# Kernel optimization log

Hardware: AMD Instinct MI355X
Metric: run time of the kernel (lower is better)

The kernel has to match this reference:

```python
import jax, jax.numpy as jnp
from jax import lax
import numpy as np

B, N, C = 64, 8732, 81  # batch, anchors (SSD300), classes (COCO+bg)
POS_RATE = 0.003        # keep 3*num_pos < N (argsort column index must be in range)


def setup_inputs() -> dict:
    key = jax.random.key(0)
    k1, k2, k3, k4, k5, k6 = jax.random.split(key, 6)
    pred_conf = jax.random.normal(k1, (B, N, C), dtype=jnp.float32)
    pred_loc = jax.random.normal(k2, (B, N, 4), dtype=jnp.float32)
    # one-hot gt_conf; class 0 = background; sparse positives
    is_pos = jax.random.uniform(k3, (B, N)) < POS_RATE
    labels = jnp.where(is_pos, jax.random.randint(k4, (B, N), 1, C), 0)
    gt_conf = jax.nn.one_hot(labels, C, dtype=jnp.float32)
    gt_loc = jax.random.normal(k5, (B, N, 4), dtype=jnp.float32)
    return {"pred_conf": pred_conf, "pred_loc": pred_loc,
            "gt_conf": gt_conf, "gt_loc": gt_loc}


def reference(pred_conf, pred_loc, gt_conf, gt_loc):
    negative_ratio = 3.0
    # softmax cross entropy per anchor: [B, N]
    log_sm = jax.nn.log_softmax(pred_conf, axis=-1)
    conf_loss = -jnp.sum(log_sm * gt_conf, axis=-1)

    # positive mask (gt background prob == 0 => positive); detached in original
    pos_mask = (lax.stop_gradient(gt_conf)[:, :, 0] == 0).astype(jnp.float32)
    num_pos = jnp.sum(pos_mask)
    positive_conf_loss = pos_mask * conf_loss

    # hard-negative mining (faithful to original, including the quirk that the
    # "threshold" is the argsort INDEX value at column num_negative_conf)
    neg_mask = 1.0 - pos_mask
    cl_neg = lax.stop_gradient(conf_loss) * neg_mask  # detached in original
    order = jnp.argsort(cl_neg, axis=-1)              # [B, N] ascending
    num_neg = (negative_ratio * num_pos).astype(jnp.int32)  # scalar, traced
    idx = jnp.broadcast_to(num_neg, (cl_neg.shape[0], 1))
    thr = jnp.take_along_axis(order, idx, axis=1).astype(jnp.float32)  # [B,1]
    neg_mask = neg_mask * (cl_neg > thr).astype(jnp.float32)
    negative_conf_loss = neg_mask * conf_loss

    conf_total = jnp.sum(positive_conf_loss + negative_conf_loss, axis=-1)  # [B]

    # smooth-L1-ish loc loss (faithful, incl. loc_loss_mask == linear mask bug)
    d = pred_loc - gt_loc
    lin = (jnp.abs(lax.stop_gradient(d)) > 1.0).astype(jnp.float32)
    loc = ((jnp.abs(d) - 0.5) * lin + 0.5 * d * d * (1.0 - lin)) * lin
    loc_total = jnp.sum(loc, axis=(-1, -2))  # [B]

    return conf_total, loc_total
```

## Files before the change

### kernel.cpp

```cpp
#include <hip/hip_runtime.h>
#include <math.h>

#define NCLS 81
#define NANCH 8732
#define NB 64
#define BUCKET_STRIDE 16
#define HSTRIDE 257
#define NLOC_BLK  2240
#define NCONF_BLK 1792
#define NTILES 17464
#define TILE_A 32
#define WAVE_F 648

__global__ __launch_bounds__(256) void conf_loc_kernel(
    const float* __restrict__ pred_conf,
    const float* __restrict__ gt_conf,
    const float* __restrict__ pred_loc,
    const float* __restrict__ gt_loc,
    float* __restrict__ cl_out,
    int* __restrict__ pos_buckets,
    float* __restrict__ row_pos,
    float* __restrict__ locp)
{
    __shared__ float sx[2][2592];
    __shared__ int labels[2][32];
    __shared__ float red[4];

    const int tid = threadIdx.x;
    const int lane = tid & 63, w = tid >> 6;

    if (blockIdx.x < NLOC_BLK) {
        const int bid = blockIdx.x;
        const int b = bid & 63;
        const int chunk = bid >> 6;
        const int idx = chunk * 256 + tid;
        float local = 0.f;
        if (idx < NANCH) {
            const float4* p = (const float4*)(pred_loc + (size_t)b * (NANCH * 4));
            const float4* g = (const float4*)(gt_loc + (size_t)b * (NANCH * 4));
            float4 pv = p[idx];
            float4 gv = g[idx];
            float a0 = fabsf(pv.x - gv.x), a1 = fabsf(pv.y - gv.y);
            float a2 = fabsf(pv.z - gv.z), a3 = fabsf(pv.w - gv.w);
            local  = (a0 > 1.f) ? (a0 - 0.5f) : 0.f;
            local += (a1 > 1.f) ? (a1 - 0.5f) : 0.f;
            local += (a2 > 1.f) ? (a2 - 0.5f) : 0.f;
            local += (a3 > 1.f) ? (a3 - 0.5f) : 0.f;
        }
        for (int off = 32; off; off >>= 1) local += __shfl_xor(local, off);
        if (lane == 0) red[w] = local;
        __syncthreads();
        if (tid == 0) locp[bid] = red[0] + red[1] + red[2] + red[3];
        return;
    }

    const int pid = blockIdx.x - NLOC_BLK;
    float* swA = &sx[0][w * WAVE_F];
    float* swB = &sx[1][w * WAVE_F];
    int pacc = 0;

#define DMA3(dst, src)                                                              \
    do {                                                                            \
        __builtin_amdgcn_global_load_lds(                                           \
            (const __attribute__((address_space(1))) unsigned int*)((src) + lane),  \
            (__attribute__((address_space(3))) unsigned int*)(&(dst)[lane * 4]),    \
            16, 0, 0);                                                              \
        __builtin_amdgcn_global_load_lds(                                           \
            (const __attribute__((address_space(1))) unsigned int*)((src) + 64 + lane), \
            (__attribute__((address_space(3))) unsigned int*)(&(dst)[(64 + lane) * 4]), \
            16, 0, 0);                                                              \
        if (lane < 34)                                                              \
            __builtin_amdgcn_global_load_lds(                                       \
                (const __attribute__((address_space(1))) unsigned int*)((src) + 128 + lane), \
                (__attribute__((address_space(3))) unsigned int*)(&(dst)[(128 + lane) * 4]), \
                16, 0, 0);                                                          \
    } while (0)

    int T = pid;
    {
        const float4* ps = (const float4*)(pred_conf + (size_t)T * 2592 + w * WAVE_F);
        DMA3(swA, ps);
    }
    const float4* gs = (const float4*)(gt_conf + (size_t)T * 2592 + w * WAVE_F);
    float4 g0 = gs[lane];
    float4 g1 = gs[64 + lane];
    float4 g2 = (lane < 34) ? gs[128 + lane] : float4{0.f, 0.f, 0.f, 0.f};

    int cur = 0;
    for (;;) {
        const int Tn = T + NCONF_BLK;
        const bool hasN = (Tn < NTILES);
        float* swc = cur ? swB : swA;
        float* swn = cur ? swA : swB;

        if (hasN) {
            const float4* ps = (const float4*)(pred_conf + (size_t)Tn * 2592 + w * WAVE_F);
            DMA3(swn, ps);
            asm volatile("s_waitcnt vmcnt(3)" ::: "memory");
        } else {
            asm volatile("s_waitcnt vmcnt(0)" ::: "memory");
        }
        __builtin_amdgcn_sched_barrier(0);

        {
            const float4 gg[3] = {g0, g1, g2};
#pragma unroll
            for (int c = 0; c < 3; ++c) {
                const int f4 = c * 64 + lane;
                float gv[4] = {gg[c].x, gg[c].y, gg[c].z, gg[c].w};
#pragma unroll
                for (int t = 0; t < 4; ++t) {
                    if (gv[t] != 0.0f) {
                        const int e = 4 * f4 + t;
                        const int a = e / 81, cls = e - 81 * a;
                        labels[cur][w * 8 + a] = cls;
                        pacc += (cls != 0);
                    }
                }
            }
        }
        if (hasN) {
            const float4* gn = (const float4*)(gt_conf + (size_t)Tn * 2592 + w * WAVE_F);
            g0 = gn[lane];
            g1 = gn[64 + lane];
            g2 = (lane < 34) ? gn[128 + lane] : float4{0.f, 0.f, 0.f, 0.f};
        }
        asm volatile("s_waitcnt lgkmcnt(0)" ::: "memory");
        __builtin_amdgcn_sched_barrier(0);

        {
            const int a = lane >> 3, r = lane & 7;
            const float* xr = swc + a * 81;
            float s = 0.f;
#pragma unroll
            for (int j = 0; j < 10; ++j) s += __expf(xr[r + 8 * j]);
            if (r == 0) s += __expf(xr[80]);
            s += __shfl_xor(s, 1);
            s += __shfl_xor(s, 2);
            s += __shfl_xor(s, 4);
            const float lse = __logf(s);

            const int anchor = T * TILE_A + w * 8 + a;
            float contrib = 0.f;
            if (r == 0) {
                const int lbl = labels[cur][w * 8 + a];
                const float cl = lse - xr[lbl];
                const bool posf = (lbl != 0);
                cl_out[anchor] = posf ? 0.0f : cl;
                if (posf) contrib = cl;
            }
            const int b = anchor / NANCH;
            const int bF = __builtin_amdgcn_readfirstlane(b);
            float c0 = (b == bF) ? contrib : 0.0f;
            float c1 = contrib - c0;
            for (int off = 32; off; off >>= 1) {
                c0 += __shfl_xor(c0, off);
                c1 += __shfl_xor(c1, off);
            }
            if (lane == 0) {
                if (c0 != 0.f) atomicAdd(&row_pos[bF], c0);
                if (c1 != 0.f) atomicAdd(&row_pos[bF + 1], c1);
            }
        }

        if (!hasN) break;
        T = Tn;
        cur ^= 1;
    }
#undef DMA3

    for (int off = 32; off; off >>= 1) pacc += __shfl_xor(pacc, off);
    if (lane == 0 && pacc)
        atomicAdd(&pos_buckets[(((pid << 2) | w) & 63) * BUCKET_STRIDE], pacc);
}

__global__ __launch_bounds__(1024) void select_kernel(
    const float* __restrict__ val,
    const int* __restrict__ pos_buckets,
    const float* __restrict__ row_pos,
    const float* __restrict__ locp,
    float* __restrict__ out)
{
    __shared__ float cl[NANCH];
    __shared__ int hist[4 * HSTRIDE];
    __shared__ int wsum[16];
    __shared__ float fred[16];
    __shared__ int sh_numpos;
    __shared__ unsigned int sh_prefix;
    __shared__ int sh_k, sh_thr;

    const int b = blockIdx.x;
    const int tid = threadIdx.x;
    const int lane = tid & 63, w = tid >> 6;
    const int hofs = (w & 3) * HSTRIDE;
    const float* row = val + b * NANCH;

    if (tid < 64) {
        int v = pos_buckets[tid * BUCKET_STRIDE];
        for (int off = 32; off; off >>= 1) v += __shfl_xor(v, off);
        if (tid == 0) sh_numpos = v;
    } else if (tid < 128) {
        float v = (lane < 35) ? locp[lane * 64 + b] : 0.f;
        for (int off = 32; off; off >>= 1) v += __shfl_xor(v, off);
        if (lane == 0) out[64 + b] = v;
    }
    for (int i = tid; i < NANCH; i += 1024) cl[i] = row[i];
    __syncthreads();

    int k = 3 * sh_numpos;
    if (k > NANCH - 1) k = NANCH - 1;
    if (k < 0) k = 0;

    unsigned int prefix = 0u;
    for (int r = 0; r < 4; ++r) {
        const int shift = 24 - 8 * r;
        const unsigned int maskHigh = (r == 0) ? 0u : (0xFFFFFFFFu << (shift + 8));
        for (int j = tid; j < 4 * HSTRIDE; j += 1024) hist[j] = 0;
        __syncthreads();
        if (r == 0) {
            for (int i0 = 0; i0 < 9216; i0 += 1024) {
                int i = i0 + tid;
                bool valid = (i < NANCH);
                unsigned int u = valid ? __float_as_uint(cl[i]) : 0u;
                int bin = (int)(u >> 24);
                unsigned long long act = __ballot(valid);
                while (act) {
                    int leader = (int)__ffsll((long long)act) - 1;
                    int lbin = __shfl(bin, leader);
                    unsigned long long sm = __ballot(valid && (bin == lbin));
                    if (lane == leader) atomicAdd(&hist[hofs + lbin], (int)__popcll(sm));
                    act &= ~sm;
                }
            }
        } else {
            for (int i = tid; i < NANCH; i += 1024) {
                unsigned int u = __float_as_uint(cl[i]);
                if ((u & maskHigh) == prefix)
                    atomicAdd(&hist[hofs + ((u >> shift) & 0xFF)], 1);
            }
        }
        __syncthreads();
        int h = 0, v = 0;
        if (tid < 256) {
            h = hist[tid] + hist[HSTRIDE + tid] + hist[2 * HSTRIDE + tid]
              + hist[3 * HSTRIDE + tid];
            v = h;
#pragma unroll
            for (int off = 1; off < 64; off <<= 1) {
                int u2 = __shfl_up(v, off);
                if (lane >= off) v += u2;
            }
            if (lane == 63) wsum[w] = v;
        }
        __syncthreads();
        if (tid < 256) {
            int add = 0;
            for (int i = 0; i < w; ++i) add += wsum[i];
            int incl = v + add, excl = incl - h;
            if (excl <= k && k < incl) {
                sh_prefix = prefix | ((unsigned int)tid << shift);
                sh_k = k - excl;
            }
        }
        __syncthreads();
        prefix = sh_prefix;
        k = sh_k;
        __syncthreads();
    }
    const unsigned int T = prefix;

    const int CHUNK = 9;
    int lo = tid * CHUNK; if (lo > NANCH) lo = NANCH;
    int hi = lo + CHUNK; if (hi > NANCH) hi = NANCH;
    int cnt = 0;
    for (int i = lo; i < hi; ++i)
        cnt += (__float_as_uint(cl[i]) == T);
    int v2 = cnt;
#pragma unroll
    for (int off = 1; off < 64; off <<= 1) {
        int u2 = __shfl_up(v2, off);
        if (lane >= off) v2 += u2;
    }
    if (lane == 63) wsum[w] = v2;
    __syncthreads();
    if (tid < 16) {
        int s = wsum[tid];
#pragma unroll
        for (int off = 1; off < 16; off <<= 1) {
            int u2 = __shfl_up(s, off);
            if (lane >= off) s += u2;
        }
        wsum[tid] = s;
    }
    __syncthreads();
    {
        int add = (w == 0) ? 0 : wsum[w - 1];
        int incl = v2 + add, excl = incl - cnt;
        if (excl <= k && k < incl) {
            int need = k - excl, idx = NANCH - 1;
            for (int i = lo; i < hi; ++i) {
                if (__float_as_uint(cl[i]) == T) {
                    if (need == 0) { idx = i; break; }
                    --need;
                }
            }
            sh_thr = idx;
        }
    }
    __syncthreads();

    const float thr = (float)sh_thr;
    float local = 0.f;
    for (int i = tid; i < NANCH; i += 1024) {
        float c = cl[i];
        if (c > thr) local += c;
    }
    for (int off = 32; off; off >>= 1) local += __shfl_xor(local, off);
    if (lane == 0) fred[w] = local;
    __syncthreads();
    if (tid == 0) {
        float t = row_pos[b];
        for (int i = 0; i < 16; ++i) t += fred[i];
        out[b] = t;
    }
}

extern "C" void kernel_launch(void* const* d_in, const int* in_sizes, int n_in,
                              void* d_out, int out_size, void* d_ws, size_t ws_size,
                              hipStream_t stream) {
    const float* pred_conf = (const float*)d_in[0];
    const float* pred_loc  = (const float*)d_in[1];
    const float* gt_conf   = (const float*)d_in[2];
    const float* gt_loc    = (const float*)d_in[3];
    float* out = (float*)d_out;

    int*   pos_buckets = (int*)d_ws;
    float* row_pos     = (float*)((char*)d_ws + 4096);
    float* locp        = (float*)((char*)d_ws + 5120);
    float* vals        = (float*)((char*)d_ws + 16384);

    hipMemsetAsync(d_ws, 0, 8192, stream);

    conf_loc_kernel<<<NLOC_BLK + NCONF_BLK, 256, 0, stream>>>(
        pred_conf, gt_conf, pred_loc, gt_loc, vals, pos_buckets, row_pos, locp);
    select_kernel<<<NB, 1024, 0, stream>>>(vals, pos_buckets, row_pos, locp, out);
}
```

Baseline: 393.3 us.

## Fuse conf/loc and selection kernels via a global completion counter

Merges the two kernel launches into one grid. The last 64 blocks spin on a global atomic done-counter until all producer blocks have finished, then run the per-row radix select with 256 threads instead of 1024. This removes one kernel launch and the gap between the two kernels. In exchange it relies on the waiting blocks not starving producers (they are scheduled last), and each selection block now has 4x fewer threads for the histogram passes.

```diff
diff --git a/kernel.cpp b/kernel.cpp
--- a/kernel.cpp
+++ b/kernel.cpp
@@ -8,11 +8,33 @@
 #define HSTRIDE 257
 #define NLOC_BLK  2240
 #define NCONF_BLK 1792
+#define NSEL_BLK  64
 #define NTILES 17464
 #define TILE_A 32
 #define WAVE_F 648
-
-__global__ __launch_bounds__(256) void conf_loc_kernel(
+#define DONE_TARGET (NLOC_BLK + NCONF_BLK)
+
+#define ALD_I(p) __hip_atomic_load((p), __ATOMIC_RELAXED, __HIP_MEMORY_SCOPE_AGENT)
+#define ALD_F(p) __hip_atomic_load((p), __ATOMIC_RELAXED, __HIP_MEMORY_SCOPE_AGENT)
+
+struct ConfSh {
+    float sx[2][2592];
+    int labels[2][32];
+    float red[4];
+};
+struct SelSh {
+    float cl[NANCH];
+    int hist[4 * HSTRIDE];
+    int wsum[4];
+    float fred[4];
+    int numpos;
+    unsigned int prefix;
+    int k;
+    int thr;
+};
+union ShMem { ConfSh c; SelSh s; };
+
+__global__ __launch_bounds__(256) void fused_kernel(
     const float* __restrict__ pred_conf,
     const float* __restrict__ gt_conf,
     const float* __restrict__ pred_loc,
@@ -20,11 +42,11 @@
     float* __restrict__ cl_out,
     int* __restrict__ pos_buckets,
     float* __restrict__ row_pos,
-    float* __restrict__ locp)
+    float* __restrict__ locp,
+    int* __restrict__ done,
+    float* __restrict__ out)
 {
-    __shared__ float sx[2][2592];
-    __shared__ int labels[2][32];
-    __shared__ float red[4];
+    __shared__ ShMem sh;
 
     const int tid = threadIdx.x;
     const int lane = tid & 63, w = tid >> 6;
@@ -48,16 +70,21 @@
             local += (a3 > 1.f) ? (a3 - 0.5f) : 0.f;
         }
         for (int off = 32; off; off >>= 1) local += __shfl_xor(local, off);
-        if (lane == 0) red[w] = local;
-        __syncthreads();
-        if (tid == 0) locp[bid] = red[0] + red[1] + red[2] + red[3];
+        if (lane == 0) sh.c.red[w] = local;
+        __syncthreads();
+        if (tid == 0) {
+            locp[bid] = sh.c.red[0] + sh.c.red[1] + sh.c.red[2] + sh.c.red[3];
+            __threadfence();
+            atomicAdd(done, 1);
+        }
         return;
     }
 
-    const int pid = blockIdx.x - NLOC_BLK;
-    float* swA = &sx[0][w * WAVE_F];
-    float* swB = &sx[1][w * WAVE_F];
-    int pacc = 0;
+    if (blockIdx.x < NLOC_BLK + NCONF_BLK) {
+        const int pid = blockIdx.x - NLOC_BLK;
+        float* swA = &sh.c.sx[0][w * WAVE_F];
+        float* swB = &sh.c.sx[1][w * WAVE_F];
+        int pacc = 0;
 
 #define DMA3(dst, src)                                                              \
     do {                                                                            \
@@ -76,149 +103,164 @@
                 16, 0, 0);                                                          \
     } while (0)
 
-    int T = pid;
-    {
-        const float4* ps = (const float4*)(pred_conf + (size_t)T * 2592 + w * WAVE_F);
-        DMA3(swA, ps);
-    }
-    const float4* gs = (const float4*)(gt_conf + (size_t)T * 2592 + w * WAVE_F);
-    float4 g0 = gs[lane];
-    float4 g1 = gs[64 + lane];
-    float4 g2 = (lane < 34) ? gs[128 + lane] : float4{0.f, 0.f, 0.f, 0.f};
-
-    int cur = 0;
-    for (;;) {
-        const int Tn = T + NCONF_BLK;
-        const bool hasN = (Tn < NTILES);
-        float* swc = cur ? swB : swA;
-        float* swn = cur ? swA : swB;
-
-        if (hasN) {
-            const float4* ps = (const float4*)(pred_conf + (size_t)Tn * 2592 + w * WAVE_F);
-            DMA3(swn, ps);
-            asm volatile("s_waitcnt vmcnt(3)" ::: "memory");
-        } else {
-            asm volatile("s_waitcnt vmcnt(0)" ::: "memory");
-        }
-        __builtin_amdgcn_sched_barrier(0);
-
+        int T = pid;
         {
-            const float4 gg[3] = {g0, g1, g2};
-#pragma unroll
-            for (int c = 0; c < 3; ++c) {
-                const int f4 = c * 64 + lane;
-                float gv[4] = {gg[c].x, gg[c].y, gg[c].z, gg[c].w};
-#pragma unroll
-                for (int t = 0; t < 4; ++t) {
-                    if (gv[t] != 0.0f) {
-                        const int e = 4 * f4 + t;
-                        const int a = e / 81, cls = e - 81 * a;
-                        labels[cur][w * 8 + a] = cls;
-                        pacc += (cls != 0);
+            const float4* ps = (const float4*)(pred_conf + (size_t)T * 2592 + w * WAVE_F);
+            DMA3(swA, ps);
+        }
+        const float4* gs = (const float4*)(gt_conf + (size_t)T * 2592 + w * WAVE_F);
+        float4 g0 = gs[lane];
+        float4 g1 = gs[64 + lane];
+        float4 g2 = (lane < 34) ? gs[128 + lane] : float4{0.f, 0.f, 0.f, 0.f};
+
+        int cur = 0;
+        for (;;) {
+            const int Tn = T + NCONF_BLK;
+            const bool hasN = (Tn < NTILES);
+            float* swc = cur ? swB : swA;
+            float* swn = cur ? swA : swB;
+
+            if (hasN) {
+                const float4* ps = (const float4*)(pred_conf + (size_t)Tn * 2592 + w * WAVE_F);
+                DMA3(swn, ps);
+                asm volatile("s_waitcnt vmcnt(3)" ::: "memory");
+            } else {
+                asm volatile("s_waitcnt vmcnt(0)" ::: "memory");
+            }
+            __builtin_amdgcn_sched_barrier(0);
+
+            {
+                const float4 gg[3] = {g0, g1, g2};
+#pragma unroll
+                for (int c = 0; c < 3; ++c) {
+                    const int f4 = c * 64 + lane;
+                    float gv[4] = {gg[c].x, gg[c].y, gg[c].z, gg[c].w};
+#pragma unroll
+                    for (int t = 0; t < 4; ++t) {
+                        if (gv[t] != 0.0f) {
+                            const int e = 4 * f4 + t;
+                            const int a = e / 81, cls = e - 81 * a;
+                            sh.c.labels[cur][w * 8 + a] = cls;
+                            pacc += (cls != 0);
+                        }
                     }
                 }
             }
-        }
-        if (hasN) {
-            const float4* gn = (const float4*)(gt_conf + (size_t)Tn * 2592 + w * WAVE_F);
-            g0 = gn[lane];
-            g1 = gn[64 + lane];
-            g2 = (lane < 34) ? gn[128 + lane] : float4{0.f, 0.f, 0.f, 0.f};
-        }
-        asm volatile("s_waitcnt lgkmcnt(0)" ::: "memory");
-        __builtin_amdgcn_sched_barrier(0);
-
-        {
-            const int a = lane >> 3, r = lane & 7;
-            const float* xr = swc + a * 81;
-            float s = 0.f;
-#pragma unroll
-            for (int j = 0; j < 10; ++j) s += __expf(xr[r + 8 * j]);
-            if (r == 0) s += __expf(xr[80]);
-            s += __shfl_xor(s, 1);
-            s += __shfl_xor(s, 2);
-            s += __shfl_xor(s, 4);
-            const float lse = __logf(s);
-
-            const int anchor = T * TILE_A + w * 8 + a;
-            float contrib = 0.f;
-            if (r == 0) {
-                const int lbl = labels[cur][w * 8 + a];
-                const float cl = lse - xr[lbl];
-                const bool posf = (lbl != 0);
-                cl_out[anchor] = posf ? 0.0f : cl;
-                if (posf) contrib = cl;
-            }
-            const int b = anchor / NANCH;
-            const int bF = __builtin_amdgcn_readfirstlane(b);
-            float c0 = (b == bF) ? contrib : 0.0f;
-            float c1 = contrib - c0;
-            for (int off = 32; off; off >>= 1) {
-                c0 += __shfl_xor(c0, off);
-                c1 += __shfl_xor(c1, off);
-            }
-            if (lane == 0) {
-                if (c0 != 0.f) atomicAdd(&row_pos[bF], c0);
-                if (c1 != 0.f) atomicAdd(&row_pos[bF + 1], c1);
-            }
-        }
-
-        if (!hasN) break;
-        T = Tn;
-        cur ^= 1;
-    }
+            if (hasN) {
+                const float4* gn = (const float4*)(gt_conf + (size_t)Tn * 2592 + w * WAVE_F);
+                g0 = gn[lane];
+                g1 = gn[64 + lane];
+                g2 = (lane < 34) ? gn[128 + lane] : float4{0.f, 0.f, 0.f, 0.f};
+            }
+            asm volatile("s_waitcnt lgkmcnt(0)" ::: "memory");
+            __builtin_amdgcn_sched_barrier(0);
+
+            {
+                const int a = lane >> 3, r = lane & 7;
+                const float* xr = swc + a * 81;
+                float s = 0.f;
+#pragma unroll
+                for (int j = 0; j < 10; ++j) s += __expf(xr[r + 8 * j]);
+                if (r == 0) s += __expf(xr[80]);
+                s += __shfl_xor(s, 1);
+                s += __shfl_xor(s, 2);
+                s += __shfl_xor(s, 4);
+                const float lse = __logf(s);
+
+                const int anchor = T * TILE_A + w * 8 + a;
+                float contrib = 0.f;
+                if (r == 0) {
+                    const int lbl = sh.c.labels[cur][w * 8 + a];
+                    const float cl = lse - xr[lbl];
+                    const bool posf = (lbl != 0);
+                    cl_out[anchor] = posf ? 0.0f : cl;
+                    if (posf) contrib = cl;
+                }
+                const int b = anchor / NANCH;
+                const int bF = __builtin_amdgcn_readfirstlane(b);
+                float c0 = (b == bF) ? contrib : 0.0f;
+                float c1 = contrib - c0;
+                for (int off = 32; off; off >>= 1) {
+                    c0 += __shfl_xor(c0, off);
+                    c1 += __shfl_xor(c1, off);
+                }
+                if (lane == 0) {
+                    if (c0 != 0.f) atomicAdd(&row_pos[bF], c0);
+                    if (c1 != 0.f) atomicAdd(&row_pos[bF + 1], c1);
+                }
+            }
+
+            if (!hasN) break;
+            T = Tn;
+            cur ^= 1;
+        }
 #undef DMA3
 
-    for (int off = 32; off; off >>= 1) pacc += __shfl_xor(pacc, off);
-    if (lane == 0 && pacc)
-        atomicAdd(&pos_buckets[(((pid << 2) | w) & 63) * BUCKET_STRIDE], pacc);
-}
-
-__global__ __launch_bounds__(1024) void select_kernel(
-    const float* __restrict__ val,
-    const int* __restrict__ pos_buckets,
-    const float* __restrict__ row_pos,
-    const float* __restrict__ locp,
-    float* __restrict__ out)
-{
-    __shared__ float cl[NANCH];
-    __shared__ int hist[4 * HSTRIDE];
-    __shared__ int wsum[16];
-    __shared__ float fred[16];
-    __shared__ int sh_numpos;
-    __shared__ unsigned int sh_prefix;
-    __shared__ int sh_k, sh_thr;
-
-    const int b = blockIdx.x;
-    const int tid = threadIdx.x;
-    const int lane = tid & 63, w = tid >> 6;
-    const int hofs = (w & 3) * HSTRIDE;
-    const float* row = val + b * NANCH;
+        for (int off = 32; off; off >>= 1) pacc += __shfl_xor(pacc, off);
+        if (lane == 0 && pacc)
+            atomicAdd(&pos_buckets[(((pid << 2) | w) & 63) * BUCKET_STRIDE], pacc);
+
+        __threadfence();
+        __syncthreads();
+        if (tid == 0) atomicAdd(done, 1);
+        return;
+    }
+
+    const int b = blockIdx.x - (NLOC_BLK + NCONF_BLK);
+
+    if (tid == 0) {
+        while (ALD_I(done) < DONE_TARGET) __builtin_amdgcn_s_sleep(8);
+    }
+    __syncthreads();
+    __threadfence();
 
     if (tid < 64) {
-        int v = pos_buckets[tid * BUCKET_STRIDE];
+        int v = ALD_I(&pos_buckets[tid * BUCKET_STRIDE]);
         for (int off = 32; off; off >>= 1) v += __shfl_xor(v, off);
-        if (tid == 0) sh_numpos = v;
+        if (tid == 0) sh.s.numpos = v;
     } else if (tid < 128) {
-        float v = (lane < 35) ? locp[lane * 64 + b] : 0.f;
+        float v = (lane < 35) ? ALD_F(&locp[lane * 64 + b]) : 0.f;
         for (int off = 32; off; off >>= 1) v += __shfl_xor(v, off);
         if (lane == 0) out[64 + b] = v;
     }
-    for (int i = tid; i < NANCH; i += 1024) cl[i] = row[i];
+
+    float* rowp = (float*)(cl_out + (size_t)b * NANCH);
+    float* cl = sh.s.cl;
+    for (int it0 = 0; it0 < 32; it0 += 8) {
+        float t[8];
+#pragma unroll
+        for (int j = 0; j < 8; ++j) t[j] = ALD_F(rowp + tid + 256 * (it0 + j));
+#pragma unroll
+        for (int j = 0; j < 8; ++j) cl[tid + 256 * (it0 + j)] = t[j];
+    }
+    {
+        float t[3];
+#pragma unroll
+        for (int j = 0; j < 3; ++j) {
+            const int i = tid + 256 * (32 + j);
+            t[j] = (i < NANCH) ? ALD_F(rowp + i) : 0.f;
+        }
+#pragma unroll
+        for (int j = 0; j < 3; ++j) {
+            const int i = tid + 256 * (32 + j);
+            if (i < NANCH) cl[i] = t[j];
+        }
+    }
     __syncthreads();
 
-    int k = 3 * sh_numpos;
+    int k = 3 * sh.s.numpos;
     if (k > NANCH - 1) k = NANCH - 1;
     if (k < 0) k = 0;
 
+    const int hofs = w * HSTRIDE;
     unsigned int prefix = 0u;
     for (int r = 0; r < 4; ++r) {
         const int shift = 24 - 8 * r;
         const unsigned int maskHigh = (r == 0) ? 0u : (0xFFFFFFFFu << (shift + 8));
-        for (int j = tid; j < 4 * HSTRIDE; j += 1024) hist[j] = 0;
+        for (int j = tid; j < 4 * HSTRIDE; j += 256) sh.s.hist[j] = 0;
         __syncthreads();
         if (r == 0) {
-            for (int i0 = 0; i0 < 9216; i0 += 1024) {
+            for (int i0 = 0; i0 < 8960; i0 += 256) {
                 int i = i0 + tid;
                 bool valid = (i < NANCH);
                 unsigned int u = valid ? __float_as_uint(cl[i]) : 0u;
@@ -228,100 +270,87 @@
                     int leader = (int)__ffsll((long long)act) - 1;
                     int lbin = __shfl(bin, leader);
                     unsigned long long sm = __ballot(valid && (bin == lbin));
-                    if (lane == leader) atomicAdd(&hist[hofs + lbin], (int)__popcll(sm));
+                    if (lane == leader) atomicAdd(&sh.s.hist[hofs + lbin], (int)__popcll(sm));
                     act &= ~sm;
                 }
             }
         } else {
-            for (int i = tid; i < NANCH; i += 1024) {
+            for (int i = tid; i < NANCH; i += 256) {
                 unsigned int u = __float_as_uint(cl[i]);
                 if ((u & maskHigh) == prefix)
-                    atomicAdd(&hist[hofs + ((u >> shift) & 0xFF)], 1);
-            }
-        }
-        __syncthreads();
-        int h = 0, v = 0;
-        if (tid < 256) {
-            h = hist[tid] + hist[HSTRIDE + tid] + hist[2 * HSTRIDE + tid]
-              + hist[3 * HSTRIDE + tid];
-            v = h;
-#pragma unroll
-            for (int off = 1; off < 64; off <<= 1) {
-                int u2 = __shfl_up(v, off);
-                if (lane >= off) v += u2;
-            }
-            if (lane == 63) wsum[w] = v;
-        }
-        __syncthreads();
-        if (tid < 256) {
+                    atomicAdd(&sh.s.hist[hofs + ((u >> shift) & 0xFF)], 1);
+            }
+        }
+        __syncthreads();
+        int h = sh.s.hist[tid] + sh.s.hist[HSTRIDE + tid]
+              + sh.s.hist[2 * HSTRIDE + tid] + sh.s.hist[3 * HSTRIDE + tid];
+        int v = h;
+#pragma unroll
+        for (int off = 1; off < 64; off <<= 1) {
+            int u2 = __shfl_up(v, off);
+            if (lane >= off) v += u2;
+        }
+        if (lane == 63) sh.s.wsum[w] = v;
+        __syncthreads();
+        {
             int add = 0;
-            for (int i = 0; i < w; ++i) add += wsum[i];
+            for (int i = 0; i < w; ++i) add += sh.s.wsum[i];
             int incl = v + add, excl = incl - h;
             if (excl <= k && k < incl) {
-                sh_prefix = prefix | ((unsigned int)tid << shift);
-                sh_k = k - excl;
-            }
-        }
-        __syncthreads();
-        prefix = sh_prefix;
-        k = sh_k;
-        __syncthreads();
-    }
-    const unsigned int T = prefix;
-
-    const int CHUNK = 9;
-    int lo = tid * CHUNK; if (lo > NANCH) lo = NANCH;
-    int hi = lo + CHUNK; if (hi > NANCH) hi = NANCH;
-    int cnt = 0;
-    for (int i = lo; i < hi; ++i)
-        cnt += (__float_as_uint(cl[i]) == T);
-    int v2 = cnt;
-#pragma unroll
-    for (int off = 1; off < 64; off <<= 1) {
-        int u2 = __shfl_up(v2, off);
-        if (lane >= off) v2 += u2;
-    }
-    if (lane == 63) wsum[w] = v2;
-    __syncthreads();
-    if (tid < 16) {
-        int s = wsum[tid];
-#pragma unroll
-        for (int off = 1; off < 16; off <<= 1) {
-            int u2 = __shfl_up(s, off);
-            if (lane >= off) s += u2;
-        }
-        wsum[tid] = s;
-    }
-    __syncthreads();
+                sh.s.prefix = prefix | ((unsigned int)tid << shift);
+                sh.s.k = k - excl;
+            }
+        }
+        __syncthreads();
+        prefix = sh.s.prefix;
+        k = sh.s.k;
+        __syncthreads();
+    }
+    const unsigned int TT = prefix;
+
     {
-        int add = (w == 0) ? 0 : wsum[w - 1];
+        const int CH = 35;
+        int lo = tid * CH; if (lo > NANCH) lo = NANCH;
+        int hi = lo + CH; if (hi > NANCH) hi = NANCH;
+        int cnt = 0;
+        for (int i = lo; i < hi; ++i)
+            cnt += (__float_as_uint(cl[i]) == TT);
+        int v2 = cnt;
+#pragma unroll
+        for (int off = 1; off < 64; off <<= 1) {
+            int u2 = __shfl_up(v2, off);
+            if (lane >= off) v2 += u2;
+        }
+        if (lane == 63) sh.s.wsum[w] = v2;
+        __syncthreads();
+        int add = 0;
+        for (int i = 0; i < w; ++i) add += sh.s.wsum[i];
         int incl = v2 + add, excl = incl - cnt;
         if (excl <= k && k < incl) {
             int need = k - excl, idx = NANCH - 1;
             for (int i = lo; i < hi; ++i) {
-                if (__float_as_uint(cl[i]) == T) {
+                if (__float_as_uint(cl[i]) == TT) {
                     if (need == 0) { idx = i; break; }
                     --need;
                 }
             }
-            sh_thr = idx;
+            sh.s.thr = idx;
         }
     }
     __syncthreads();
 
-    const float thr = (float)sh_thr;
+    const float thr = (float)sh.s.thr;
     float local = 0.f;
-    for (int i = tid; i < NANCH; i += 1024) {
+    for (int i = tid; i < NANCH; i += 256) {
         float c = cl[i];
         if (c > thr) local += c;
     }
     for (int off = 32; off; off >>= 1) local += __shfl_xor(local, off);
-    if (lane == 0) fred[w] = local;
+    if (lane == 0) sh.s.fred[w] = local;
     __syncthreads();
     if (tid == 0) {
-        float t = row_pos[b];
-        for (int i = 0; i < 16; ++i) t += fred[i];
-        out[b] = t;
+        float t = ALD_F(&row_pos[b]);
+        out[b] = t + sh.s.fred[0] + sh.s.fred[1] + sh.s.fred[2] + sh.s.fred[3];
     }
 }
 
@@ -336,12 +365,13 @@
 
     int*   pos_buckets = (int*)d_ws;
     float* row_pos     = (float*)((char*)d_ws + 4096);
+    int*   done        = (int*)((char*)d_ws + 4608);
     float* locp        = (float*)((char*)d_ws + 5120);
     float* vals        = (float*)((char*)d_ws + 16384);
 
     hipMemsetAsync(d_ws, 0, 8192, stream);
 
-    conf_loc_kernel<<<NLOC_BLK + NCONF_BLK, 256, 0, stream>>>(
-        pred_conf, gt_conf, pred_loc, gt_loc, vals, pos_buckets, row_pos, locp);
-    select_kernel<<<NB, 1024, 0, stream>>>(vals, pos_buckets, row_pos, locp, out);
+    fused_kernel<<<NLOC_BLK + NCONF_BLK + NSEL_BLK, 256, 0, stream>>>(
+        pred_conf, gt_conf, pred_loc, gt_loc, vals, pos_buckets, row_pos,
+        locp, done, out);
 }
```

Measured after the change: 752.3 us. 1.91x slower.
